# Kernel tuning notes

Measured on AMD Instinct MI355X. Metric: run time of the kernel, lower is better.

## Reference

```python
import jax, jax.numpy as jnp
import numpy as np

N, E, DIN, HID, DOUT = 50000, 800000, 128, 128, 64
NEG_SLOPE = 0.2


def setup_inputs() -> dict:
    key = jax.random.key(0)
    ks = jax.random.split(key, 16)
    x = jax.random.normal(ks[0], (N, DIN), dtype=jnp.float32)
    edge_index = jax.random.randint(ks[1], (2, E), 0, N, dtype=jnp.int64)

    def lin(k, fan_in, fan_out):
        kw, kb = jax.random.split(k)
        s = 1.0 / np.sqrt(fan_in)
        W = jax.random.uniform(kw, (fan_in, fan_out), jnp.float32, -s, s)
        b = jax.random.uniform(kb, (fan_out,), jnp.float32, -s, s)
        return W, b

    Wl, bl = lin(ks[2], DIN, DIN)   # GATv2 lin_l
    Wr, br = lin(ks[3], DIN, DIN)   # GATv2 lin_r
    att = jax.random.uniform(ks[4], (DIN,), jnp.float32, -1.0 / np.sqrt(DIN), 1.0 / np.sqrt(DIN))
    bg = jnp.zeros((DIN,), jnp.float32)  # GAT output bias
    W1, b1 = lin(ks[5], DIN, HID)   # ChebConv K=1 -> plain linear
    W2, b2 = lin(ks[6], HID, HID)
    W3, b3 = lin(ks[7], HID, DOUT)
    return {"x": x, "edge_index": edge_index, "Wl": Wl, "bl": bl, "Wr": Wr,
            "br": br, "att": att, "bg": bg, "W1": W1, "b1": b1,
            "W2": W2, "b2": b2, "W3": W3, "b3": b3}


def reference(x, edge_index, Wl, bl, Wr, br, att, bg, W1, b1, W2, b2, W3, b3):
    n = x.shape[0]
    # GATv2Conv adds self loops by default
    loop = jnp.arange(n, dtype=edge_index.dtype)
    src = jnp.concatenate([edge_index[0], loop])  # source j
    dst = jnp.concatenate([edge_index[1], loop])  # target i

    xl = x @ Wl + bl  # [N, DIN]
    xr = x @ Wr + br  # [N, DIN]

    # GATv2 edge scores: leaky_relu(x_l[j] + x_r[i]) . att
    e = jax.nn.leaky_relu(xl[src] + xr[dst], NEG_SLOPE)  # [E+N, DIN]
    a = e @ att                                          # [E+N]

    # softmax over incoming edges of each destination node
    amax = jax.ops.segment_max(a, dst, num_segments=n)
    ea = jnp.exp(a - amax[dst])
    denom = jax.ops.segment_sum(ea, dst, num_segments=n)
    alpha = ea / denom[dst]                              # [E+N]

    # aggregate messages alpha * x_l[j] at destinations
    h = jax.ops.segment_sum(alpha[:, None] * xl[src], dst, num_segments=n) + bg

    # ChebConv with K=1 reduces to a linear layer (T_0(L) = I)
    h = jax.nn.relu(h @ W1 + b1)
    h = jax.nn.relu(h @ W2 + b2)
    # dropout_rate = 0.0 -> identity
    return h @ W3 + b3
```

## Files before the change

kernel.cpp:

```cpp
#include <hip/hip_runtime.h>
#include <hip/hip_bf16.h>

#define DIN 128
#define NEG_SLOPE 0.2f
#define PTILE 2048
#define FCAP 8192
#define CVT_BLKS 289

typedef __attribute__((ext_vector_type(8))) short bf16x8;
typedef __attribute__((ext_vector_type(8))) unsigned short u16x8;
typedef __attribute__((ext_vector_type(4))) float f32x4;
typedef __attribute__((ext_vector_type(2))) float f32x2;
typedef __attribute__((ext_vector_type(4))) unsigned int u32x4;

__device__ __forceinline__ ushort f2bf(float f) {
  unsigned u = __float_as_uint(f);
  u += 0x7FFFu + ((u >> 16) & 1u);
  return (ushort)(u >> 16);
}
__device__ __forceinline__ float bf2f(ushort u) {
  return __uint_as_float((unsigned)u << 16);
}
__device__ __forceinline__ f32x2 bfpair(unsigned u) {
  f32x2 r;
  r.x = __uint_as_float(u << 16);
  r.y = __uint_as_float(u & 0xFFFF0000u);
  return r;
}

template <int CTRL>
__device__ __forceinline__ float dppadd(float x) {
  int v = __builtin_amdgcn_update_dpp(0, __float_as_int(x), CTRL, 0xf, 0xf, true);
  return x + __int_as_float(v);
}
__device__ __forceinline__ float red16(float t) {
  t = dppadd<0xB1>(t);
  t = dppadd<0x4E>(t);
  t = dppadd<0x141>(t);
  t = dppadd<0x140>(t);
  return t;
}

__global__ __launch_bounds__(256) void cvt_hist_kernel(
    const float* __restrict__ Wl, const float* __restrict__ Wr,
    const float* __restrict__ W1, const float* __restrict__ W2,
    const float* __restrict__ W3,
    ushort* __restrict__ WlT, ushort* __restrict__ WrT,
    ushort* __restrict__ W1T, ushort* __restrict__ W2T,
    ushort* __restrict__ W3T,
    const int* __restrict__ ei, int* __restrict__ ghist, int E) {
  if (blockIdx.x < CVT_BLKS) {
    int i = blockIdx.x * 256 + threadIdx.x;
    if (i < 16384) {
      int k = i >> 7, c = i & 127; WlT[c * 128 + k] = f2bf(Wl[i]);
    } else if (i < 32768) {
      int j = i - 16384; int k = j >> 7, c = j & 127; WrT[c * 128 + k] = f2bf(Wr[j]);
    } else if (i < 49152) {
      int j = i - 32768; int k = j >> 7, c = j & 127; W1T[c * 128 + k] = f2bf(W1[j]);
    } else if (i < 65536) {
      int j = i - 49152; int k = j >> 7, c = j & 127; W2T[c * 128 + k] = f2bf(W2[j]);
    } else if (i < 73728) {
      int j = i - 65536; int k = j >> 6, c = j & 63; W3T[c * 128 + k] = f2bf(W3[j]);
    }
  } else {
    __shared__ int h[256];
    h[threadIdx.x] = 0;
    __syncthreads();
    int tile = blockIdx.x - CVT_BLKS;
    for (int e = tile * PTILE + threadIdx.x;
         e < min(E, (tile + 1) * PTILE); e += 256)
      atomicAdd(&h[ei[E + e] >> 8], 1);
    __syncthreads();
    if (h[threadIdx.x] > 0) atomicAdd(&ghist[threadIdx.x], h[threadIdx.x]);
  }
}

__global__ __launch_bounds__(256) void scan_small_kernel(
    const int* __restrict__ ghist, int* __restrict__ cum,
    int* __restrict__ cursor) {
  __shared__ int sh[256];
  int tid = threadIdx.x;
  int v = ghist[tid];
  sh[tid] = v;
  __syncthreads();
  for (int d = 1; d < 256; d <<= 1) {
    int t = (tid >= d) ? sh[tid - d] : 0;
    __syncthreads();
    sh[tid] += t;
    __syncthreads();
  }
  int exc = sh[tid] - v;
  cum[tid] = exc;
  cursor[tid] = exc;
  if (tid == 255) cum[256] = sh[255];
}

__global__ __launch_bounds__(256) void lin_partition_kernel(
    const float* __restrict__ x,
    const ushort* __restrict__ WlT, const float* __restrict__ bl,
    const ushort* __restrict__ WrT, const float* __restrict__ br,
    ushort* __restrict__ xl, ushort* __restrict__ xr, int n, int nblk_lin,
    const int* __restrict__ ei, unsigned* __restrict__ part,
    int* __restrict__ cursor, int E) {
  if ((int)blockIdx.x < nblk_lin) {
    const int tid = threadIdx.x;
    const int wv = tid >> 6, lane = tid & 63;
    const int m = lane & 15, quad = lane >> 4;
    const int colbase = (wv & 1) * 64;
    const int nodew = blockIdx.x * 32 + (wv >> 1) * 16;
    int arow = nodew + m; if (arow >= n) arow = n - 1;
    f32x4 accl[4], accr[4];
#pragma unroll
    for (int nt = 0; nt < 4; nt++) { accl[nt] = (f32x4){0,0,0,0}; accr[nt] = (f32x4){0,0,0,0}; }
#pragma unroll
    for (int kk = 0; kk < 4; kk++) {
      int k0 = kk * 32 + quad * 8;
      const float4* xp = (const float4*)(x + (long)arow * 128 + k0);
      float4 x0 = xp[0], x1 = xp[1];
      bf16x8 af;
      af[0] = (short)f2bf(x0.x); af[1] = (short)f2bf(x0.y);
      af[2] = (short)f2bf(x0.z); af[3] = (short)f2bf(x0.w);
      af[4] = (short)f2bf(x1.x); af[5] = (short)f2bf(x1.y);
      af[6] = (short)f2bf(x1.z); af[7] = (short)f2bf(x1.w);
#pragma unroll
      for (int nt = 0; nt < 4; nt++) {
        int brow = colbase + nt * 16 + m;
        bf16x8 bl8 = *(const bf16x8*)(WlT + brow * 128 + k0);
        bf16x8 br8 = *(const bf16x8*)(WrT + brow * 128 + k0);
        accl[nt] = __builtin_amdgcn_mfma_f32_16x16x32_bf16(af, bl8, accl[nt], 0, 0, 0);
        accr[nt] = __builtin_amdgcn_mfma_f32_16x16x32_bf16(af, br8, accr[nt], 0, 0, 0);
      }
    }
#pragma unroll
    for (int nt = 0; nt < 4; nt++) {
      int col = colbase + nt * 16 + m;
      float vbl = bl[col], vbr = br[col];
#pragma unroll
      for (int r = 0; r < 4; r++) {
        int node = nodew + quad * 4 + r;
        if (node < n) {
          xl[(long)node * 128 + col] = f2bf(accl[nt][r] + vbl);
          xr[(long)node * 128 + col] = f2bf(accr[nt][r] + vbr);
        }
      }
    }
  } else {
    __shared__ int hist[256], pref[256], sexcl[256], curs[256], gbase[256];
    __shared__ unsigned buf[PTILE];
    const int tid = threadIdx.x;
    const int tile0 = ((int)blockIdx.x - nblk_lin) * PTILE;
    const int tcount = min(PTILE, E - tile0);
    hist[tid] = 0;
    __syncthreads();
    unsigned pk[PTILE / 256];
    int cnt = 0;
    for (int i = tid; i < tcount; i += 256) {
      int e = tile0 + i;
      int s = ei[e], d = ei[E + e];
      unsigned p = ((unsigned)d << 16) | (unsigned)s;
      pk[cnt++] = p;
      atomicAdd(&hist[d >> 8], 1);
    }
    __syncthreads();
    int v = hist[tid];
    pref[tid] = v;
    __syncthreads();
    for (int d = 1; d < 256; d <<= 1) {
      int t = (tid >= d) ? pref[tid - d] : 0;
      __syncthreads();
      pref[tid] += t;
      __syncthreads();
    }
    int exc = pref[tid] - v;
    sexcl[tid] = exc;
    curs[tid] = exc;
    gbase[tid] = (v > 0) ? atomicAdd(&cursor[tid], v) : 0;
    __syncthreads();
    for (int j = 0; j < cnt; j++) {
      int b = pk[j] >> 24;
      int pos = atomicAdd(&curs[b], 1);
      buf[pos] = pk[j];
    }
    __syncthreads();
    for (int i = tid; i < tcount; i += 256) {
      unsigned p = buf[i];
      int b = p >> 24;
      part[gbase[b] + (i - sexcl[b])] = p;
    }
  }
}

__global__ __launch_bounds__(512) void fine_kernel(
    const unsigned* __restrict__ part, const int* __restrict__ cum,
    int* __restrict__ offsets, ushort* __restrict__ ssrc,
    int N, int E, int nbuck) {
  __shared__ int hist[256], pref[256], curs[256];
  __shared__ unsigned buf[FCAP], buf2[FCAP];
  const int tid = threadIdx.x;
  const int b = blockIdx.x;
  const int seg0 = cum[b];
  const int len = min(cum[b + 1] - seg0, FCAP);
  if (tid < 256) hist[tid] = 0;
  __syncthreads();
  for (int i = tid; i < len; i += 512) {
    unsigned p = part[seg0 + i];
    buf[i] = p;
    atomicAdd(&hist[(p >> 16) & 255], 1);
  }
  __syncthreads();
  int v = (tid < 256) ? hist[tid] : 0;
  if (tid < 256) pref[tid] = v;
  __syncthreads();
  for (int d = 1; d < 256; d <<= 1) {
    int t = (tid >= d && tid < 256) ? pref[tid - d] : 0;
    __syncthreads();
    if (tid < 256) pref[tid] += t;
    __syncthreads();
  }
  if (tid < 256) {
    int exc = pref[tid] - v;
    curs[tid] = exc;
    int node = b * 256 + tid;
    if (node < N) offsets[node] = seg0 + exc;
  }
  if (b == nbuck - 1 && tid == 0) offsets[N] = E;
  __syncthreads();
  for (int i = tid; i < len; i += 512) {
    unsigned p = buf[i];
    int pos = atomicAdd(&curs[(p >> 16) & 255], 1);
    buf2[pos] = p;
  }
  __syncthreads();
  for (int i = tid; i < len; i += 512)
    ssrc[seg0 + i] = (ushort)(buf2[i] & 0xFFFFu);
}

__global__ __launch_bounds__(256) void node_aggr_kernel(
    const ushort* __restrict__ xl, const ushort* __restrict__ xr,
    const float* __restrict__ att, const float* __restrict__ bg,
    const int* __restrict__ offsets, const ushort* __restrict__ ssrc,
    ushort* __restrict__ h, int n) {
  int wave = (int)((blockIdx.x * (long)blockDim.x + threadIdx.x) >> 6);
  int lane = threadIdx.x & 63;
  if (wave >= n) return;
  const int node = wave;
  const int eg = lane >> 4, sl = lane & 15;
  f32x2 av2[4], r2[4], acc2[4];
  {
    const float4* ap = (const float4*)(att + sl * 8);
    float4 a0 = ap[0], a1 = ap[1];
    av2[0] = (f32x2){a0.x, a0.y}; av2[1] = (f32x2){a0.z, a0.w};
    av2[2] = (f32x2){a1.x, a1.y}; av2[3] = (f32x2){a1.z, a1.w};
  }
  const ushort* __restrict__ xls = xl + sl * 8;
  u32x4 rv = *(const u32x4*)(xr + (long)node * 128 + sl * 8);
  u32x4 lv = *(const u32x4*)(xls + (long)node * 128);
  float denom;
  {
    f32x2 t2 = {0.f, 0.f};
    f32x2 l2[4];
#pragma unroll
    for (int jp = 0; jp < 4; jp++) {
      r2[jp] = bfpair(rv[jp]);
      l2[jp] = bfpair(lv[jp]);
      f32x2 v = l2[jp] + r2[jp];
      t2 += __builtin_elementwise_max(v, NEG_SLOPE * v) * av2[jp];
    }
    float t = red16(t2.x + t2.y);
    float es = __expf(t);
    denom = (eg == 0) ? es : 0.f;
#pragma unroll
    for (int jp = 0; jp < 4; jp++)
      acc2[jp] = (eg == 0) ? es * l2[jp] : (f32x2){0.f, 0.f};
  }
  const int beg = offsets[node];
  const int end = offsets[node + 1];
  int ia = beg + 2 * eg;
  bool va = ia < end, vb = ia + 1 < end;
  int sa = va ? (int)ssrc[ia] : node;
  int sb = vb ? (int)ssrc[ia + 1] : node;
  u32x4 uva = *(const u32x4*)(xls + (long)sa * 128);
  u32x4 uvb = *(const u32x4*)(xls + (long)sb * 128);
  for (int p = beg; p < end; p += 8) {
    u32x4 ca = uva, cb = uvb;
    bool cva = va, cvb = vb;
    int ian = p + 8 + 2 * eg;
    va = ian < end; vb = ian + 1 < end;
    sa = va ? (int)ssrc[ian] : node;
    sb = vb ? (int)ssrc[ian + 1] : node;
    uva = *(const u32x4*)(xls + (long)sa * 128);
    uvb = *(const u32x4*)(xls + (long)sb * 128);
    f32x2 ua2[4], ub2[4];
    f32x2 ta2 = {0.f, 0.f}, tb2 = {0.f, 0.f};
#pragma unroll
    for (int jp = 0; jp < 4; jp++) {
      ua2[jp] = bfpair(ca[jp]);
      ub2[jp] = bfpair(cb[jp]);
      f32x2 va2 = ua2[jp] + r2[jp];
      f32x2 vb2 = ub2[jp] + r2[jp];
      ta2 += __builtin_elementwise_max(va2, NEG_SLOPE * va2) * av2[jp];
      tb2 += __builtin_elementwise_max(vb2, NEG_SLOPE * vb2) * av2[jp];
    }
    float ta = red16(ta2.x + ta2.y);
    float tb = red16(tb2.x + tb2.y);
    float ea = cva ? __expf(ta) : 0.f;
    float eb = cvb ? __expf(tb) : 0.f;
    denom += ea + eb;
#pragma unroll
    for (int jp = 0; jp < 4; jp++)
      acc2[jp] += ea * ua2[jp] + eb * ub2[jp];
  }
#pragma unroll
  for (int jp = 0; jp < 4; jp++) {
    acc2[jp].x += __shfl_xor(acc2[jp].x, 16);
    acc2[jp].y += __shfl_xor(acc2[jp].y, 16);
    acc2[jp].x += __shfl_xor(acc2[jp].x, 32);
    acc2[jp].y += __shfl_xor(acc2[jp].y, 32);
  }
  denom += __shfl_xor(denom, 16);
  denom += __shfl_xor(denom, 32);
  if (eg == 0) {
    float inv = 1.0f / denom;
    const float4* bp = (const float4*)(bg + sl * 8);
    float4 g0 = bp[0], g1 = bp[1];
    f32x2 gv[4] = {{g0.x, g0.y}, {g0.z, g0.w}, {g1.x, g1.y}, {g1.z, g1.w}};
    u16x8 o;
#pragma unroll
    for (int jp = 0; jp < 4; jp++) {
      f32x2 hv = acc2[jp] * inv + gv[jp];
      o[2 * jp]     = f2bf(hv.x);
      o[2 * jp + 1] = f2bf(hv.y);
    }
    *(u16x8*)(h + (long)node * 128 + sl * 8) = o;
  }
}

#define LDSP 136
__global__ __launch_bounds__(256) void mlp_mfma_kernel(
    const ushort* __restrict__ hb,
    const ushort* __restrict__ W1T, const float* __restrict__ b1,
    const ushort* __restrict__ W2T, const float* __restrict__ b2,
    const ushort* __restrict__ W3T, const float* __restrict__ b3,
    float* __restrict__ out, int n) {
  __shared__ ushort act[32][LDSP];
  const int tid = threadIdx.x;
  const int wv = tid >> 6, lane = tid & 63;
  const int m = lane & 15, quad = lane >> 4;
  const int half = wv & 1, ng = wv >> 1;
  const int colbase = half * 64;
  const int nodew = blockIdx.x * 32 + ng * 16;
  int arow = nodew + m; if (arow >= n) arow = n - 1;
  f32x4 acc[4];
#pragma unroll
  for (int nt = 0; nt < 4; nt++) acc[nt] = (f32x4){0,0,0,0};
#pragma unroll
  for (int kk = 0; kk < 4; kk++) {
    int k0 = kk * 32 + quad * 8;
    bf16x8 af = *(const bf16x8*)(hb + (long)arow * 128 + k0);
#pragma unroll
    for (int nt = 0; nt < 4; nt++) {
      bf16x8 b8 = *(const bf16x8*)(W1T + (colbase + nt * 16 + m) * 128 + k0);
      acc[nt] = __builtin_amdgcn_mfma_f32_16x16x32_bf16(af, b8, acc[nt], 0, 0, 0);
    }
  }
#pragma unroll
  for (int nt = 0; nt < 4; nt++) {
    int col = colbase + nt * 16 + m;
    float b = b1[col];
#pragma unroll
    for (int r = 0; r < 4; r++)
      act[ng * 16 + quad * 4 + r][col] = f2bf(fmaxf(acc[nt][r] + b, 0.f));
  }
  __syncthreads();
#pragma unroll
  for (int nt = 0; nt < 4; nt++) acc[nt] = (f32x4){0,0,0,0};
#pragma unroll
  for (int kk = 0; kk < 4; kk++) {
    int k0 = kk * 32 + quad * 8;
    bf16x8 af = *(const bf16x8*)(&act[ng * 16 + m][k0]);
#pragma unroll
    for (int nt = 0; nt < 4; nt++) {
      bf16x8 b8 = *(const bf16x8*)(W2T + (colbase + nt * 16 + m) * 128 + k0);
      acc[nt] = __builtin_amdgcn_mfma_f32_16x16x32_bf16(af, b8, acc[nt], 0, 0, 0);
    }
  }
  __syncthreads();
#pragma unroll
  for (int nt = 0; nt < 4; nt++) {
    int col = colbase + nt * 16 + m;
    float b = b2[col];
#pragma unroll
    for (int r = 0; r < 4; r++)
      act[ng * 16 + quad * 4 + r][col] = f2bf(fmaxf(acc[nt][r] + b, 0.f));
  }
  __syncthreads();
  f32x4 acc3[2];
#pragma unroll
  for (int nt = 0; nt < 2; nt++) acc3[nt] = (f32x4){0,0,0,0};
#pragma unroll
  for (int kk = 0; kk < 4; kk++) {
    int k0 = kk * 32 + quad * 8;
    bf16x8 af = *(const bf16x8*)(&act[ng * 16 + m][k0]);
#pragma unroll
    for (int nt = 0; nt < 2; nt++) {
      bf16x8 b8 = *(const bf16x8*)(W3T + (half * 32 + nt * 16 + m) * 128 + k0);
      acc3[nt] = __builtin_amdgcn_mfma_f32_16x16x32_bf16(af, b8, acc3[nt], 0, 0, 0);
    }
  }
#pragma unroll
  for (int nt = 0; nt < 2; nt++) {
    int col = half * 32 + nt * 16 + m;
    float b = b3[col];
#pragma unroll
    for (int r = 0; r < 4; r++) {
      int node = nodew + quad * 4 + r;
      if (node < n) out[(long)node * 64 + col] = acc3[nt][r] + b;
    }
  }
}

extern "C" void kernel_launch(void* const* d_in, const int* in_sizes, int n_in,
                              void* d_out, int out_size, void* d_ws, size_t ws_size,
                              hipStream_t stream) {
  const float* x   = (const float*)d_in[0];
  const int*   ei  = (const int*)d_in[1];
  const float* Wl  = (const float*)d_in[2];
  const float* bl  = (const float*)d_in[3];
  const float* Wr  = (const float*)d_in[4];
  const float* br  = (const float*)d_in[5];
  const float* att = (const float*)d_in[6];
  const float* bg  = (const float*)d_in[7];
  const float* W1  = (const float*)d_in[8];
  const float* b1  = (const float*)d_in[9];
  const float* W2  = (const float*)d_in[10];
  const float* b2  = (const float*)d_in[11];
  const float* W3  = (const float*)d_in[12];
  const float* b3  = (const float*)d_in[13];
  float* out = (float*)d_out;

  const int N = in_sizes[0] / DIN;
  const int E = in_sizes[1] / 2;
  const int nbuck = (N + 255) >> 8;

  char* ws = (char*)d_ws;
  size_t off = 0;
  auto alloc = [&](size_t bytes) {
    void* p = ws + off;
    off += (bytes + 255) & ~(size_t)255;
    return p;
  };
  int* ghist     = (int*)alloc(256 * 4);
  int* cum       = (int*)alloc(257 * 4);
  int* cursor    = (int*)alloc(256 * 4);
  int* offsets   = (int*)alloc(((size_t)N + 4) * 4);
  unsigned* part = (unsigned*)alloc((size_t)E * 4);
  ushort* ssrc   = (ushort*)alloc(((size_t)E + 16) * 2);
  ushort* xlb    = (ushort*)alloc((size_t)N * DIN * 2);
  ushort* xrb    = (ushort*)alloc((size_t)N * DIN * 2);
  ushort* hbf    = (ushort*)alloc((size_t)N * DIN * 2);
  ushort* WlT    = (ushort*)alloc(16384 * 2);
  ushort* WrT    = (ushort*)alloc(16384 * 2);
  ushort* W1T    = (ushort*)alloc(16384 * 2);
  ushort* W2T    = (ushort*)alloc(16384 * 2);
  ushort* W3T    = (ushort*)alloc(8192 * 2);
  (void)ws_size;

  hipMemsetAsync(ghist, 0, 256 * 4, stream);

  int ntile = (E + PTILE - 1) / PTILE;
  cvt_hist_kernel<<<CVT_BLKS + ntile, 256, 0, stream>>>(
      Wl, Wr, W1, W2, W3, WlT, WrT, W1T, W2T, W3T, ei, ghist, E);

  scan_small_kernel<<<1, 256, 0, stream>>>(ghist, cum, cursor);

  int nblk32 = (N + 31) / 32;
  lin_partition_kernel<<<nblk32 + ntile, 256, 0, stream>>>(
      x, WlT, bl, WrT, br, xlb, xrb, N, nblk32, ei, part, cursor, E);

  fine_kernel<<<nbuck, 512, 0, stream>>>(part, cum, offsets, ssrc, N, E, nbuck);

  int nwblk = (N + 3) / 4;
  node_aggr_kernel<<<nwblk, 256, 0, stream>>>(xlb, xrb, att, bg,
                                              offsets, ssrc, hbf, N);

  mlp_mfma_kernel<<<nblk32, 256, 0, stream>>>(hbf, W1T, b1, W2T, b2,
                                              W3T, b3, out, N);
}
```

Measured before the change: 238.2 us.

## Replace two-level radix partition with per-node histogram CSR and atomic scatter

Drops the bucket partition and fine-sort kernels. The CSR is now built from a per-node degree histogram in global memory, a three-kernel scan over nodes, and a direct atomic scatter of source ids into ssrc fused with the linear layer. This removes the intermediate packed edge array and the shared-memory sort passes, at the cost of many global atomics and a nondeterministic edge order within each node. The aggregation kernel also rewrites leaky_relu as 0.6*v + 0.4*|v| folded into the attention weights, and clamps prefetch indices instead of using selects.

```diff
diff --git a/kernel.cpp b/kernel.cpp
--- a/kernel.cpp
+++ b/kernel.cpp
@@ -4,7 +4,6 @@
 #define DIN 128
 #define NEG_SLOPE 0.2f
 #define PTILE 2048
-#define FCAP 8192
 #define CVT_BLKS 289
 
 typedef __attribute__((ext_vector_type(8))) short bf16x8;
@@ -17,9 +16,6 @@
   unsigned u = __float_as_uint(f);
   u += 0x7FFFu + ((u >> 16) & 1u);
   return (ushort)(u >> 16);
-}
-__device__ __forceinline__ float bf2f(ushort u) {
-  return __uint_as_float((unsigned)u << 16);
 }
 __device__ __forceinline__ f32x2 bfpair(unsigned u) {
   f32x2 r;
@@ -48,7 +44,7 @@
     ushort* __restrict__ WlT, ushort* __restrict__ WrT,
     ushort* __restrict__ W1T, ushort* __restrict__ W2T,
     ushort* __restrict__ W3T,
-    const int* __restrict__ ei, int* __restrict__ ghist, int E) {
+    const int* __restrict__ ei, int* __restrict__ nhist, int E) {
   if (blockIdx.x < CVT_BLKS) {
     int i = blockIdx.x * 256 + threadIdx.x;
     if (i < 16384) {
@@ -63,24 +59,21 @@
       int j = i - 65536; int k = j >> 6, c = j & 63; W3T[c * 128 + k] = f2bf(W3[j]);
     }
   } else {
-    __shared__ int h[256];
-    h[threadIdx.x] = 0;
-    __syncthreads();
-    int tile = blockIdx.x - CVT_BLKS;
-    for (int e = tile * PTILE + threadIdx.x;
-         e < min(E, (tile + 1) * PTILE); e += 256)
-      atomicAdd(&h[ei[E + e] >> 8], 1);
-    __syncthreads();
-    if (h[threadIdx.x] > 0) atomicAdd(&ghist[threadIdx.x], h[threadIdx.x]);
-  }
-}
-
-__global__ __launch_bounds__(256) void scan_small_kernel(
-    const int* __restrict__ ghist, int* __restrict__ cum,
-    int* __restrict__ cursor) {
+    int tile = (int)blockIdx.x - CVT_BLKS;
+    int base = tile * PTILE;
+    int lim = min(E, base + PTILE);
+    for (int e = base + threadIdx.x; e < lim; e += 256)
+      atomicAdd(&nhist[ei[E + e]], 1);
+  }
+}
+
+__global__ __launch_bounds__(256) void scanA_kernel(
+    const int* __restrict__ nhist, int* __restrict__ offsets,
+    int* __restrict__ bsum, int N) {
   __shared__ int sh[256];
   int tid = threadIdx.x;
-  int v = ghist[tid];
+  int node = blockIdx.x * 256 + tid;
+  int v = (node < N) ? nhist[node] : 0;
   sh[tid] = v;
   __syncthreads();
   for (int d = 1; d < 256; d <<= 1) {
@@ -89,19 +82,46 @@
     sh[tid] += t;
     __syncthreads();
   }
-  int exc = sh[tid] - v;
-  cum[tid] = exc;
-  cursor[tid] = exc;
-  if (tid == 255) cum[256] = sh[255];
-}
-
-__global__ __launch_bounds__(256) void lin_partition_kernel(
+  if (node < N) offsets[node] = sh[tid] - v;
+  if (tid == 255) bsum[blockIdx.x] = sh[255];
+}
+
+__global__ __launch_bounds__(256) void scanB_kernel(
+    const int* __restrict__ bsum, int* __restrict__ gbase,
+    int* __restrict__ offsets, int N, int nbuck, int E) {
+  __shared__ int sh[256];
+  int tid = threadIdx.x;
+  int v = (tid < nbuck) ? bsum[tid] : 0;
+  sh[tid] = v;
+  __syncthreads();
+  for (int d = 1; d < 256; d <<= 1) {
+    int t = (tid >= d) ? sh[tid - d] : 0;
+    __syncthreads();
+    sh[tid] += t;
+    __syncthreads();
+  }
+  if (tid < nbuck) gbase[tid] = sh[tid] - v;
+  if (tid == 0) offsets[N] = E;
+}
+
+__global__ __launch_bounds__(256) void scanC_kernel(
+    int* __restrict__ offsets, const int* __restrict__ gbase,
+    int* __restrict__ cursor, int N) {
+  int node = blockIdx.x * 256 + threadIdx.x;
+  if (node < N) {
+    int o = offsets[node] + gbase[blockIdx.x];
+    offsets[node] = o;
+    cursor[node] = o;
+  }
+}
+
+__global__ __launch_bounds__(256) void lin_scatter_kernel(
     const float* __restrict__ x,
     const ushort* __restrict__ WlT, const float* __restrict__ bl,
     const ushort* __restrict__ WrT, const float* __restrict__ br,
     ushort* __restrict__ xl, ushort* __restrict__ xr, int n, int nblk_lin,
-    const int* __restrict__ ei, unsigned* __restrict__ part,
-    int* __restrict__ cursor, int E) {
+    const int* __restrict__ ei, int* __restrict__ cursor,
+    ushort* __restrict__ ssrc, int E) {
   if ((int)blockIdx.x < nblk_lin) {
     const int tid = threadIdx.x;
     const int wv = tid >> 6, lane = tid & 63;
@@ -145,94 +165,15 @@
       }
     }
   } else {
-    __shared__ int hist[256], pref[256], sexcl[256], curs[256], gbase[256];
-    __shared__ unsigned buf[PTILE];
-    const int tid = threadIdx.x;
-    const int tile0 = ((int)blockIdx.x - nblk_lin) * PTILE;
-    const int tcount = min(PTILE, E - tile0);
-    hist[tid] = 0;
-    __syncthreads();
-    unsigned pk[PTILE / 256];
-    int cnt = 0;
-    for (int i = tid; i < tcount; i += 256) {
-      int e = tile0 + i;
+    int tile = (int)blockIdx.x - nblk_lin;
+    int base = tile * PTILE;
+    int lim = min(E, base + PTILE);
+    for (int e = base + threadIdx.x; e < lim; e += 256) {
       int s = ei[e], d = ei[E + e];
-      unsigned p = ((unsigned)d << 16) | (unsigned)s;
-      pk[cnt++] = p;
-      atomicAdd(&hist[d >> 8], 1);
-    }
-    __syncthreads();
-    int v = hist[tid];
-    pref[tid] = v;
-    __syncthreads();
-    for (int d = 1; d < 256; d <<= 1) {
-      int t = (tid >= d) ? pref[tid - d] : 0;
-      __syncthreads();
-      pref[tid] += t;
-      __syncthreads();
-    }
-    int exc = pref[tid] - v;
-    sexcl[tid] = exc;
-    curs[tid] = exc;
-    gbase[tid] = (v > 0) ? atomicAdd(&cursor[tid], v) : 0;
-    __syncthreads();
-    for (int j = 0; j < cnt; j++) {
-      int b = pk[j] >> 24;
-      int pos = atomicAdd(&curs[b], 1);
-      buf[pos] = pk[j];
-    }
-    __syncthreads();
-    for (int i = tid; i < tcount; i += 256) {
-      unsigned p = buf[i];
-      int b = p >> 24;
-      part[gbase[b] + (i - sexcl[b])] = p;
-    }
-  }
-}
-
-__global__ __launch_bounds__(512) void fine_kernel(
-    const unsigned* __restrict__ part, const int* __restrict__ cum,
-    int* __restrict__ offsets, ushort* __restrict__ ssrc,
-    int N, int E, int nbuck) {
-  __shared__ int hist[256], pref[256], curs[256];
-  __shared__ unsigned buf[FCAP], buf2[FCAP];
-  const int tid = threadIdx.x;
-  const int b = blockIdx.x;
-  const int seg0 = cum[b];
-  const int len = min(cum[b + 1] - seg0, FCAP);
-  if (tid < 256) hist[tid] = 0;
-  __syncthreads();
-  for (int i = tid; i < len; i += 512) {
-    unsigned p = part[seg0 + i];
-    buf[i] = p;
-    atomicAdd(&hist[(p >> 16) & 255], 1);
-  }
-  __syncthreads();
-  int v = (tid < 256) ? hist[tid] : 0;
-  if (tid < 256) pref[tid] = v;
-  __syncthreads();
-  for (int d = 1; d < 256; d <<= 1) {
-    int t = (tid >= d && tid < 256) ? pref[tid - d] : 0;
-    __syncthreads();
-    if (tid < 256) pref[tid] += t;
-    __syncthreads();
-  }
-  if (tid < 256) {
-    int exc = pref[tid] - v;
-    curs[tid] = exc;
-    int node = b * 256 + tid;
-    if (node < N) offsets[node] = seg0 + exc;
-  }
-  if (b == nbuck - 1 && tid == 0) offsets[N] = E;
-  __syncthreads();
-  for (int i = tid; i < len; i += 512) {
-    unsigned p = buf[i];
-    int pos = atomicAdd(&curs[(p >> 16) & 255], 1);
-    buf2[pos] = p;
-  }
-  __syncthreads();
-  for (int i = tid; i < len; i += 512)
-    ssrc[seg0 + i] = (ushort)(buf2[i] & 0xFFFFu);
+      int pos = atomicAdd(&cursor[d], 1);
+      ssrc[pos] = (ushort)s;
+    }
+  }
 }
 
 __global__ __launch_bounds__(256) void node_aggr_kernel(
@@ -245,64 +186,74 @@
   if (wave >= n) return;
   const int node = wave;
   const int eg = lane >> 4, sl = lane & 15;
-  f32x2 av2[4], r2[4], acc2[4];
+  const int beg = offsets[node];
+  const int end = offsets[node + 1];
+  const int last = end - 1;
+  const ushort* __restrict__ xls = xl + sl * 8;
+  int ia = beg + 2 * eg;
+  bool va = ia < end, vb = ia + 1 < end;
+  int sa = (int)ssrc[min(ia, last)];
+  int sb = (int)ssrc[min(ia + 1, last)];
+  u32x4 uva = *(const u32x4*)(xls + (long)sa * 128);
+  u32x4 uvb = *(const u32x4*)(xls + (long)sb * 128);
+
+  f32x2 a06[4], a04[4], r2[4], acc2[4];
   {
     const float4* ap = (const float4*)(att + sl * 8);
     float4 a0 = ap[0], a1 = ap[1];
-    av2[0] = (f32x2){a0.x, a0.y}; av2[1] = (f32x2){a0.z, a0.w};
-    av2[2] = (f32x2){a1.x, a1.y}; av2[3] = (f32x2){a1.z, a1.w};
-  }
-  const ushort* __restrict__ xls = xl + sl * 8;
+    f32x2 av[4] = {{a0.x, a0.y}, {a0.z, a0.w}, {a1.x, a1.y}, {a1.z, a1.w}};
+#pragma unroll
+    for (int jp = 0; jp < 4; jp++) {
+      a06[jp] = 0.6f * av[jp];
+      a04[jp] = 0.4f * av[jp];
+    }
+  }
   u32x4 rv = *(const u32x4*)(xr + (long)node * 128 + sl * 8);
   u32x4 lv = *(const u32x4*)(xls + (long)node * 128);
   float denom;
   {
-    f32x2 t2 = {0.f, 0.f};
+    f32x2 t1 = {0.f, 0.f}, t2 = {0.f, 0.f};
     f32x2 l2[4];
 #pragma unroll
     for (int jp = 0; jp < 4; jp++) {
       r2[jp] = bfpair(rv[jp]);
       l2[jp] = bfpair(lv[jp]);
       f32x2 v = l2[jp] + r2[jp];
-      t2 += __builtin_elementwise_max(v, NEG_SLOPE * v) * av2[jp];
-    }
-    float t = red16(t2.x + t2.y);
+      t1 += a06[jp] * v;
+      t2 += a04[jp] * __builtin_elementwise_abs(v);
+    }
+    float t = red16(t1.x + t1.y + t2.x + t2.y);
     float es = __expf(t);
     denom = (eg == 0) ? es : 0.f;
 #pragma unroll
     for (int jp = 0; jp < 4; jp++)
       acc2[jp] = (eg == 0) ? es * l2[jp] : (f32x2){0.f, 0.f};
   }
-  const int beg = offsets[node];
-  const int end = offsets[node + 1];
-  int ia = beg + 2 * eg;
-  bool va = ia < end, vb = ia + 1 < end;
-  int sa = va ? (int)ssrc[ia] : node;
-  int sb = vb ? (int)ssrc[ia + 1] : node;
-  u32x4 uva = *(const u32x4*)(xls + (long)sa * 128);
-  u32x4 uvb = *(const u32x4*)(xls + (long)sb * 128);
   for (int p = beg; p < end; p += 8) {
     u32x4 ca = uva, cb = uvb;
     bool cva = va, cvb = vb;
     int ian = p + 8 + 2 * eg;
     va = ian < end; vb = ian + 1 < end;
-    sa = va ? (int)ssrc[ian] : node;
-    sb = vb ? (int)ssrc[ian + 1] : node;
+    sa = (int)ssrc[min(ian, last)];
+    sb = (int)ssrc[min(ian + 1, last)];
     uva = *(const u32x4*)(xls + (long)sa * 128);
     uvb = *(const u32x4*)(xls + (long)sb * 128);
     f32x2 ua2[4], ub2[4];
-    f32x2 ta2 = {0.f, 0.f}, tb2 = {0.f, 0.f};
+    f32x2 ta1 = {0.f, 0.f}, ta2 = {0.f, 0.f};
+    f32x2 tb1 = {0.f, 0.f}, tb2 = {0.f, 0.f};
 #pragma unroll
     for (int jp = 0; jp < 4; jp++) {
       ua2[jp] = bfpair(ca[jp]);
       ub2[jp] = bfpair(cb[jp]);
       f32x2 va2 = ua2[jp] + r2[jp];
       f32x2 vb2 = ub2[jp] + r2[jp];
-      ta2 += __builtin_elementwise_max(va2, NEG_SLOPE * va2) * av2[jp];
-      tb2 += __builtin_elementwise_max(vb2, NEG_SLOPE * vb2) * av2[jp];
-    }
-    float ta = red16(ta2.x + ta2.y);
-    float tb = red16(tb2.x + tb2.y);
+      ta1 += a06[jp] * va2;
+      ta2 += a04[jp] * __builtin_elementwise_abs(va2);
+      tb1 += a06[jp] * vb2;
+      tb2 += a04[jp] * __builtin_elementwise_abs(vb2);
+    }
+    float ta = red16(ta1.x + ta1.y + ta2.x + ta2.y);
+    float tb = red16(tb1.x + tb1.y + tb2.x + tb2.y);
     float ea = cva ? __expf(ta) : 0.f;
     float eb = cvb ? __expf(tb) : 0.f;
     denom += ea + eb;
@@ -449,11 +400,11 @@
     off += (bytes + 255) & ~(size_t)255;
     return p;
   };
-  int* ghist     = (int*)alloc(256 * 4);
-  int* cum       = (int*)alloc(257 * 4);
-  int* cursor    = (int*)alloc(256 * 4);
+  int* bsum      = (int*)alloc(256 * 4);
+  int* gbase     = (int*)alloc(256 * 4);
+  int* nhist     = (int*)alloc((size_t)N * 4);
+  int* cursor    = (int*)alloc((size_t)N * 4);
   int* offsets   = (int*)alloc(((size_t)N + 4) * 4);
-  unsigned* part = (unsigned*)alloc((size_t)E * 4);
   ushort* ssrc   = (ushort*)alloc(((size_t)E + 16) * 2);
   ushort* xlb    = (ushort*)alloc((size_t)N * DIN * 2);
   ushort* xrb    = (ushort*)alloc((size_t)N * DIN * 2);
@@ -465,19 +416,19 @@
   ushort* W3T    = (ushort*)alloc(8192 * 2);
   (void)ws_size;
 
-  hipMemsetAsync(ghist, 0, 256 * 4, stream);
+  hipMemsetAsync(nhist, 0, (size_t)N * 4, stream);
 
   int ntile = (E + PTILE - 1) / PTILE;
   cvt_hist_kernel<<<CVT_BLKS + ntile, 256, 0, stream>>>(
-      Wl, Wr, W1, W2, W3, WlT, WrT, W1T, W2T, W3T, ei, ghist, E);
-
-  scan_small_kernel<<<1, 256, 0, stream>>>(ghist, cum, cursor);
+      Wl, Wr, W1, W2, W3, WlT, WrT, W1T, W2T, W3T, ei, nhist, E);
+
+  scanA_kernel<<<nbuck, 256, 0, stream>>>(nhist, offsets, bsum, N);
+  scanB_kernel<<<1, 256, 0, stream>>>(bsum, gbase, offsets, N, nbuck, E);
+  scanC_kernel<<<nbuck, 256, 0, stream>>>(offsets, gbase, cursor, N);
 
   int nblk32 = (N + 31) / 32;
-  lin_partition_kernel<<<nblk32 + ntile, 256, 0, stream>>>(
-      x, WlT, bl, WrT, br, xlb, xrb, N, nblk32, ei, part, cursor, E);
-
-  fine_kernel<<<nbuck, 512, 0, stream>>>(part, cum, offsets, ssrc, N, E, nbuck);
+  lin_scatter_kernel<<<nblk32 + ntile, 256, 0, stream>>>(
+      x, WlT, bl, WrT, br, xlb, xrb, N, nblk32, ei, cursor, ssrc, E);
 
   int nwblk = (N + 3) / 4;
   node_aggr_kernel<<<nwblk, 256, 0, stream>>>(xlb, xrb, att, bg,
```

Result: slower. 283.6 us (+19.1%).
